# Optimization experiments

Hardware: AMD Instinct MI355X
Metric: run time of the kernel (lower is better)

## Reference

```python
import jax, jax.numpy as jnp
import numpy as np

N = 10000           # nodes
E = 160000          # edges
MUL = 128           # multiplicity of each irrep (128x0e + 128x1o)
EDGE_FEAT = 8       # radial embedding dim
AVG_NUM_NEIGHBORS = 16.0
MLP_IN = MUL + MUL + EDGE_FEAT + 1  # 265
NUM_W = 4 * MUL     # irreps_mid num_irreps = 256x0e + 256x1o -> 512 path weights
SQ3 = float(np.sqrt(3.0))


def setup_inputs() -> dict:
    key = jax.random.key(0)
    ks = jax.random.split(key, 16)
    node_feats = jax.random.normal(ks[0], (N, 4 * MUL), dtype=jnp.float32)  # [N,512] = 128x0e ++ 128x1o
    edge_attrs = jax.random.normal(ks[1], (E, 4), dtype=jnp.float32)        # 1x0e ++ 1x1o
    edge_feats = jax.random.normal(ks[2], (E, EDGE_FEAT), dtype=jnp.float32)
    lengths = jax.random.uniform(ks[3], (E, 1), dtype=jnp.float32)
    edge_index = jax.random.randint(ks[4], (2, E), 0, N, dtype=jnp.int32)
    # e3nn Linear weights (stored unit-variance; forward applies 1/sqrt(fan_in))
    W_scalar = jax.random.normal(ks[5], (MUL, MUL), dtype=jnp.float32)
    W_up0 = jax.random.normal(ks[6], (MUL, MUL), dtype=jnp.float32)
    W_up1 = jax.random.normal(ks[7], (MUL, MUL), dtype=jnp.float32)
    # conv_tp_weights MLP (flax Dense: fan-scaled init, bias on first two layers)
    W1 = jax.random.normal(ks[8], (MLP_IN, MUL), dtype=jnp.float32) / np.sqrt(MLP_IN)
    b1 = jnp.zeros((MUL,), dtype=jnp.float32)
    W2 = jax.random.normal(ks[9], (MUL, MUL), dtype=jnp.float32) / np.sqrt(MUL)
    b2 = jnp.zeros((MUL,), dtype=jnp.float32)
    W3 = jax.random.normal(ks[10], (MUL, NUM_W), dtype=jnp.float32) / np.sqrt(MUL)
    # final e3nn Linear: 256x0e+256x1o -> 128x0e+128x1o
    Wout0 = jax.random.normal(ks[11], (2 * MUL, MUL), dtype=jnp.float32)
    Wout1 = jax.random.normal(ks[12], (2 * MUL, MUL), dtype=jnp.float32)
    return {"node_feats": node_feats, "edge_attrs": edge_attrs, "edge_feats": edge_feats,
            "lengths": lengths, "edge_index": edge_index, "W_scalar": W_scalar,
            "W_up0": W_up0, "W_up1": W_up1, "W1": W1, "b1": b1, "W2": W2, "b2": b2,
            "W3": W3, "Wout0": Wout0, "Wout1": Wout1}


def reference(node_feats, edge_attrs, edge_feats, lengths, edge_index,
              W_scalar, W_up0, W_up1, W1, b1, W2, b2, W3, Wout0, Wout1):
    n = node_feats.shape[0]
    inv = 1.0 / np.sqrt(MUL)
    x0 = node_feats[:, :MUL]                       # [N,128]   0e
    x1 = node_feats[:, MUL:].reshape(n, MUL, 3)    # [N,128,3] 1o

    # linear_scalar: only 0e->0e path survives
    scalars = (x0 @ W_scalar) * inv                # [N,128]
    # linear_up: per-irrep channel mixing
    h0 = (x0 @ W_up0) * inv                        # [N,128]
    h1 = jnp.einsum('nmi,mo->noi', x1, W_up1) * inv  # [N,128,3]

    sender, receiver = edge_index[0], edge_index[1]

    # conv_tp_weights MLP
    mlp_in = jnp.concatenate([scalars[sender], scalars[receiver], edge_feats, lengths], axis=-1)
    h = jax.nn.silu(mlp_in @ W1 + b1)
    h = jax.nn.silu(h @ W2 + b2)
    tpw = h @ W3                                   # [E,512]

    xs0 = h0[sender]                               # [E,128]
    xs1 = h1[sender]                               # [E,128,3]
    y0 = edge_attrs[:, 0:1]                        # [E,1]  0e
    y1 = edge_attrs[:, 1:4]                        # [E,3]  1o

    # CG tensor product (component normalization), filtered to {0e,1o}; sorted order:
    # 0e block = [0e*0e->0e, 1o*1o->0e], 1o block = [0e*1o->1o, 1o*0e->1o]
    mA = xs0 * y0                                       # [E,128]   0e
    mD = (xs1 * y1[:, None, :]).sum(-1) / SQ3           # [E,128]   0e
    mB = xs0[:, :, None] * y1[:, None, :]               # [E,128,3] 1o
    mC = xs1 * y0[:, :, None]                           # [E,128,3] 1o

    # per-irrep path weights (one scalar per irrep channel)
    wA, wD = tpw[:, :MUL], tpw[:, MUL:2 * MUL]
    wB, wC = tpw[:, 2 * MUL:3 * MUL], tpw[:, 3 * MUL:]

    m0 = jnp.concatenate([mA * wA, mD * wD], axis=1)                          # [E,256]
    m1 = jnp.concatenate([mB * wB[:, :, None], mC * wC[:, :, None]], axis=1)  # [E,256,3]

    # scatter-sum aggregation to receivers
    agg0 = jax.ops.segment_sum(m0, receiver, num_segments=n)  # [N,256]
    agg1 = jax.ops.segment_sum(m1, receiver, num_segments=n)  # [N,256,3]

    # final e3nn Linear + / avg_num_neighbors
    scale = 1.0 / (np.sqrt(2 * MUL) * AVG_NUM_NEIGHBORS)
    out0 = (agg0 @ Wout0) * scale                             # [N,128]
    out1 = jnp.einsum('nmi,mo->noi', agg1, Wout1) * scale     # [N,128,3]

    # reshape_irreps: [N, mul, sum(ir dims)] = [N,128,4]
    return jnp.concatenate([out0[:, :, None], out1], axis=-1)
```

## Files before the change

### kernel.cpp

```cpp
#include <hip/hip_runtime.h>
#include <hip/hip_bf16.h>

#define NN 10000
#define NE 160000
#define TILE 32
#define A1S 264
#define A2S 136

typedef __attribute__((ext_vector_type(8))) short short8;
typedef __attribute__((ext_vector_type(4))) float f32x4;

__device__ __forceinline__ float silu_f(float x) { return x / (1.0f + __expf(-x)); }
__device__ __forceinline__ unsigned short bf16u(float v) {
    __hip_bfloat16 b = __float2bfloat16(v);
    return *reinterpret_cast<unsigned short*>(&b);
}
__device__ __forceinline__ short8 pack8(float4 a, float4 b) {
    short8 r;
    r[0]=(short)bf16u(a.x); r[1]=(short)bf16u(a.y); r[2]=(short)bf16u(a.z); r[3]=(short)bf16u(a.w);
    r[4]=(short)bf16u(b.x); r[5]=(short)bf16u(b.y); r[6]=(short)bf16u(b.z); r[7]=(short)bf16u(b.w);
    return r;
}
__device__ __forceinline__ void lds_barrier() {
    asm volatile("s_waitcnt lgkmcnt(0)" ::: "memory");
    __builtin_amdgcn_s_barrier();
    asm volatile("" ::: "memory");
}

#define OFF_W1  0
#define OFF_W2  36864
#define OFF_W3  53248
#define OFF_WSC 118784
#define OFF_WU0 135168
#define OFF_WU1 151552
#define OFF_WO0 167936
#define OFF_WO1 200704
#define WP_TOTAL 233472

__global__ __launch_bounds__(256) void convert_weights(
    const float* __restrict__ W1, const float* __restrict__ W2,
    const float* __restrict__ W3, const float* __restrict__ Wsc,
    const float* __restrict__ Wu0, const float* __restrict__ Wu1,
    const float* __restrict__ Wo0, const float* __restrict__ Wo1,
    unsigned short* __restrict__ wp,
    const int* __restrict__ edge_index, int* __restrict__ deg)
{
    int idx = blockIdx.x * 256 + threadIdx.x;
    if (idx < NE) atomicAdd(&deg[edge_index[NE + idx]], 1);
    if (idx >= WP_TOTAL) return;
    const float* src; int off, N, K;
    if      (idx < OFF_W2)  { src = W1;  off = OFF_W1;  N = 128; K = 265; }
    else if (idx < OFF_W3)  { src = W2;  off = OFF_W2;  N = 128; K = 128; }
    else if (idx < OFF_WSC) { src = W3;  off = OFF_W3;  N = 512; K = 128; }
    else if (idx < OFF_WU0) { src = Wsc; off = OFF_WSC; N = 128; K = 128; }
    else if (idx < OFF_WU1) { src = Wu0; off = OFF_WU0; N = 128; K = 128; }
    else if (idx < OFF_WO0) { src = Wu1; off = OFF_WU1; N = 128; K = 128; }
    else if (idx < OFF_WO1) { src = Wo0; off = OFF_WO0; N = 128; K = 256; }
    else                    { src = Wo1; off = OFF_WO1; N = 128; K = 256; }
    int j = idx - off;
    int kt = j / (N * 32);
    int rem = j % (N * 32);
    int n = rem >> 5, kk = rem & 31;
    int k = kt * 32 + kk;
    wp[idx] = (k < K) ? bf16u(src[k * N + n]) : (unsigned short)0;
}

__global__ __launch_bounds__(256) void node_transform(
    const float* __restrict__ node_feats,
    const unsigned short* __restrict__ wp,
    unsigned short* __restrict__ scalars_bf,
    unsigned short* __restrict__ hall,
    float* __restrict__ agg0, float* __restrict__ agg1t)
{
    __shared__ unsigned short xls[4 * 16 * 136];
    const int t = threadIdx.x;
    const int bn = blockIdx.x * 16;

    {
        const float4 z = make_float4(0.f, 0.f, 0.f, 0.f);
        float4* a0 = (float4*)(agg0 + (size_t)bn * 256);
        #pragma unroll
        for (int i = 0; i < 4; ++i) a0[t + 256 * i] = z;
        #pragma unroll
        for (int c = 0; c < 3; ++c) {
            float4* a1 = (float4*)(agg1t + (size_t)c * NN * 256 + (size_t)bn * 256);
            #pragma unroll
            for (int i = 0; i < 4; ++i) a1[t + 256 * i] = z;
        }
    }

    for (int i = t; i < 16 * 512; i += 256) {
        int n = i >> 9, j = i & 511;
        unsigned short u = bf16u(node_feats[(size_t)(bn + n) * 512 + j]);
        if (j < 128) xls[n * 136 + j] = u;
        else {
            int jj = j - 128;
            int m = jj / 3;
            int c = jj - 3 * m;
            xls[(1 + c) * 2176 + n * 136 + m] = u;
        }
    }
    __syncthreads();

    const int wv = t >> 6, lane = t & 63, l16 = lane & 15, l4 = lane >> 4;
    const unsigned short* Wscp = wp + OFF_WSC;
    const unsigned short* Wu0p = wp + OFF_WU0;
    const unsigned short* Wu1p = wp + OFF_WU1;

    f32x4 asc[2] = {}, ah0[2] = {}, ah1[3][2] = {};
    for (int kt = 0; kt < 4; ++kt) {
        short8 ax0 = *(const short8*)(xls + l16 * 136 + kt * 32 + l4 * 8);
        short8 ax1[3];
        #pragma unroll
        for (int c = 0; c < 3; ++c)
            ax1[c] = *(const short8*)(xls + (1 + c) * 2176 + l16 * 136 + kt * 32 + l4 * 8);
        #pragma unroll
        for (int n = 0; n < 2; ++n) {
            int col = wv * 32 + n * 16 + l16;
            short8 bsc = *(const short8*)(Wscp + ((size_t)kt * 128 + col) * 32 + l4 * 8);
            short8 bu0 = *(const short8*)(Wu0p + ((size_t)kt * 128 + col) * 32 + l4 * 8);
            short8 bu1 = *(const short8*)(Wu1p + ((size_t)kt * 128 + col) * 32 + l4 * 8);
            asc[n] = __builtin_amdgcn_mfma_f32_16x16x32_bf16(ax0, bsc, asc[n], 0, 0, 0);
            ah0[n] = __builtin_amdgcn_mfma_f32_16x16x32_bf16(ax0, bu0, ah0[n], 0, 0, 0);
            #pragma unroll
            for (int c = 0; c < 3; ++c)
                ah1[c][n] = __builtin_amdgcn_mfma_f32_16x16x32_bf16(ax1[c], bu1, ah1[c][n], 0, 0, 0);
        }
    }
    const float inv = 0.08838834764831845f;
    #pragma unroll
    for (int n = 0; n < 2; ++n) {
        int col = wv * 32 + n * 16 + l16;
        #pragma unroll
        for (int r = 0; r < 4; ++r) {
            int node = bn + l4 * 4 + r;
            scalars_bf[(size_t)node * 128 + col] = bf16u(asc[n][r] * inv);
            unsigned int lo = (unsigned int)bf16u(ah0[n][r] * inv)
                            | ((unsigned int)bf16u(ah1[0][n][r] * inv) << 16);
            unsigned int hi = (unsigned int)bf16u(ah1[1][n][r] * inv)
                            | ((unsigned int)bf16u(ah1[2][n][r] * inv) << 16);
            *(uint2*)(hall + ((size_t)node * 128 + col) * 4) = make_uint2(lo, hi);
        }
    }
}

__global__ __launch_bounds__(1024) void scan_kernel(const int* __restrict__ deg,
                                                    int* __restrict__ cursor) {
    __shared__ int s[1024];
    const int t = threadIdx.x;
    const int base = t * 10;
    int ld[10];
    int lsum = 0;
    #pragma unroll
    for (int i = 0; i < 10; ++i) {
        int idx = base + i;
        ld[i] = (idx < NN) ? deg[idx] : 0;
        lsum += ld[i];
    }
    s[t] = lsum;
    __syncthreads();
    for (int off = 1; off < 1024; off <<= 1) {
        int u = (t >= off) ? s[t - off] : 0;
        __syncthreads();
        s[t] += u;
        __syncthreads();
    }
    int run = s[t] - lsum;
    #pragma unroll
    for (int i = 0; i < 10; ++i) {
        int idx = base + i;
        if (idx < NN) cursor[idx] = run;
        run += ld[i];
    }
}

__global__ __launch_bounds__(256) void perm_kernel(const int* __restrict__ edge_index,
                                                   int* __restrict__ cursor,
                                                   int* __restrict__ perm) {
    int e = blockIdx.x * 256 + threadIdx.x;
    if (e < NE) {
        int r = edge_index[NE + e];
        int pos = atomicAdd(&cursor[r], 1);
        perm[pos] = e;
    }
}

__global__ __launch_bounds__(256, 6) void edge_kernel(
    const unsigned short* __restrict__ scalars_bf,
    const unsigned short* __restrict__ hall,
    const float* __restrict__ edge_attrs,
    const float* __restrict__ edge_feats,
    const float* __restrict__ lengths,
    const int* __restrict__ edge_index,
    const int* __restrict__ perm,
    const float* __restrict__ b1, const float* __restrict__ b2,
    const unsigned short* __restrict__ wp,
    float* __restrict__ agg0, float* __restrict__ agg1t)
{
    __shared__ unsigned char smem_u[25600];
    __shared__ int   eid_s[TILE];
    __shared__ int   s_s[TILE];
    __shared__ int   r_s[TILE];
    __shared__ float4 y_s[TILE];

    unsigned short* A1 = (unsigned short*)smem_u;
    unsigned short* A2 = (unsigned short*)(smem_u + 16896);
    unsigned short* A3 = A1;
    float* PKh = (float*)(smem_u + 8704);

    const int t = threadIdx.x;
    const int e0 = blockIdx.x * TILE;
    const int wv = t >> 6;
    const int lane = t & 63;
    const int l16 = lane & 15;
    const int l4 = lane >> 4;

    if (t < TILE) {
        int eid = perm[e0 + t];
        eid_s[t] = eid;
        s_s[t] = edge_index[eid];
        r_s[t] = edge_index[NE + eid];
        y_s[t] = *(const float4*)(edge_attrs + (size_t)eid * 4);
    }
    __syncthreads();

    {
        const int e = t >> 3, j = t & 7;
        const unsigned short* srow = scalars_bf + (size_t)s_s[e] * 128;
        const unsigned short* rrow = scalars_bf + (size_t)r_s[e] * 128;
        *(uint4*)(A1 + e*A1S + j*16)       = *(const uint4*)(srow + j*16);
        *(uint4*)(A1 + e*A1S + j*16 + 8)   = *(const uint4*)(srow + j*16 + 8);
        *(uint4*)(A1 + e*A1S + 128 + j*16)     = *(const uint4*)(rrow + j*16);
        *(uint4*)(A1 + e*A1S + 128 + j*16 + 8) = *(const uint4*)(rrow + j*16 + 8);
    }

    short8 ef0 = (short8){0,0,0,0,0,0,0,0}, ef1 = ef0;
    {
        int eA = l16, eB = 16 + l16;
        if (l4 == 0) {
            float4 v0 = *(const float4*)(edge_feats + (size_t)eid_s[eA] * 8);
            float4 v1 = *(const float4*)(edge_feats + (size_t)eid_s[eA] * 8 + 4);
            ef0 = pack8(v0, v1);
            float4 u0 = *(const float4*)(edge_feats + (size_t)eid_s[eB] * 8);
            float4 u1 = *(const float4*)(edge_feats + (size_t)eid_s[eB] * 8 + 4);
            ef1 = pack8(u0, u1);
        } else if (l4 == 1) {
            ef0[0] = (short)bf16u(lengths[eid_s[eA]]);
            ef1[0] = (short)bf16u(lengths[eid_s[eB]]);
        }
    }

    const int q = t >> 6, o = t & 63;
    const int rlo = q * 8;
    uint2 pfA[8], pfB[8];
    #pragma unroll
    for (int i = 0; i < 8; ++i)
        pfA[i] = *(const uint2*)(hall + ((size_t)s_s[rlo + i] * 128 + o) * 4);
    __syncthreads();

    const unsigned short* Wp1 = wp + OFF_W1;
    const unsigned short* Wp2 = wp + OFF_W2;
    const unsigned short* Wp3 = wp + OFF_W3;

    {
        f32x4 acc[2][2] = {};
        for (int kt = 0; kt < 8; ++kt) {
            short8 a0 = *(const short8*)(A1 + (     l16)*A1S + kt*32 + l4*8);
            short8 a1 = *(const short8*)(A1 + (16 + l16)*A1S + kt*32 + l4*8);
            #pragma unroll
            for (int n = 0; n < 2; ++n) {
                int col = (2*wv + n)*16 + l16;
                short8 b = *(const short8*)(Wp1 + ((size_t)kt*128 + col)*32 + l4*8);
                acc[0][n] = __builtin_amdgcn_mfma_f32_16x16x32_bf16(a0, b, acc[0][n], 0, 0, 0);
                acc[1][n] = __builtin_amdgcn_mfma_f32_16x16x32_bf16(a1, b, acc[1][n], 0, 0, 0);
            }
        }
        {
            #pragma unroll
            for (int n = 0; n < 2; ++n) {
                int col = (2*wv + n)*16 + l16;
                short8 b = *(const short8*)(Wp1 + ((size_t)8*128 + col)*32 + l4*8);
                acc[0][n] = __builtin_amdgcn_mfma_f32_16x16x32_bf16(ef0, b, acc[0][n], 0, 0, 0);
                acc[1][n] = __builtin_amdgcn_mfma_f32_16x16x32_bf16(ef1, b, acc[1][n], 0, 0, 0);
            }
        }
        #pragma unroll
        for (int n = 0; n < 2; ++n) {
            int col = (2*wv + n)*16 + l16;
            float bb = b1[col];
            #pragma unroll
            for (int m = 0; m < 2; ++m)
                #pragma unroll
                for (int r = 0; r < 4; ++r) {
                    int row = m*16 + l4*4 + r;
                    A2[row*A2S + col] = bf16u(silu_f(acc[m][n][r] + bb));
                }
        }
    }
    __syncthreads();

    {
        f32x4 acc[2][2] = {};
        for (int kt = 0; kt < 4; ++kt) {
            short8 a0 = *(const short8*)(A2 + (     l16)*A2S + kt*32 + l4*8);
            short8 a1 = *(const short8*)(A2 + (16 + l16)*A2S + kt*32 + l4*8);
            #pragma unroll
            for (int n = 0; n < 2; ++n) {
                int col = (2*wv + n)*16 + l16;
                short8 b = *(const short8*)(Wp2 + ((size_t)kt*128 + col)*32 + l4*8);
                acc[0][n] = __builtin_amdgcn_mfma_f32_16x16x32_bf16(a0, b, acc[0][n], 0, 0, 0);
                acc[1][n] = __builtin_amdgcn_mfma_f32_16x16x32_bf16(a1, b, acc[1][n], 0, 0, 0);
            }
        }
        #pragma unroll
        for (int n = 0; n < 2; ++n) {
            int col = (2*wv + n)*16 + l16;
            float bb = b2[col];
            #pragma unroll
            for (int m = 0; m < 2; ++m)
                #pragma unroll
                for (int r = 0; r < 4; ++r) {
                    int row = m*16 + l4*4 + r;
                    A3[row*A2S + col] = bf16u(silu_f(acc[m][n][r] + bb));
                }
        }
    }
    __syncthreads();

    const float rs3 = 0.57735026918962576f;
    auto do_seg = [&](const int pass, const int hh, const uint2* pf) {
        const int base0 = pass ? 128 : 0;
        const int base1 = pass ? 384 : 256;
        f32x4 acc[2][2] = {};
        for (int kt = 0; kt < 4; ++kt) {
            short8 a0 = *(const short8*)(A3 + (     l16)*A2S + kt*32 + l4*8);
            short8 a1 = *(const short8*)(A3 + (16 + l16)*A2S + kt*32 + l4*8);
            #pragma unroll
            for (int fam = 0; fam < 2; ++fam) {
                int col = (fam ? base1 : base0) + hh*64 + wv*16 + l16;
                short8 b = *(const short8*)(Wp3 + ((size_t)kt*512 + col)*32 + l4*8);
                acc[fam][0] = __builtin_amdgcn_mfma_f32_16x16x32_bf16(a0, b, acc[fam][0], 0, 0, 0);
                acc[fam][1] = __builtin_amdgcn_mfma_f32_16x16x32_bf16(a1, b, acc[fam][1], 0, 0, 0);
            }
        }
        #pragma unroll
        for (int fam = 0; fam < 2; ++fam)
            #pragma unroll
            for (int m = 0; m < 2; ++m)
                #pragma unroll
                for (int r = 0; r < 4; ++r) {
                    int row = m*16 + l4*4 + r;
                    float y0 = y_s[row].x;
                    float fold = (fam == 0) ? (pass ? rs3 : y0) : (pass ? y0 : 1.0f);
                    PKh[row*132 + fam*64 + wv*16 + l16] = acc[fam][m][r] * fold;
                }
        lds_barrier();

        {
            const int ocol = hh*64 + o;
            float ac0 = 0.f, ac1 = 0.f, ac2 = 0.f, ac3 = 0.f;
            int run_start = rlo;
            int prev_rn = r_s[rlo];

            auto flush = [&](int rn, bool interior) {
                size_t b0 = (size_t)rn * 256 + base0 + ocol;
                if (interior) {
                    agg0[b0] = ac0;
                    agg1t[0*(size_t)NN*256 + b0] = ac1;
                    agg1t[1*(size_t)NN*256 + b0] = ac2;
                    agg1t[2*(size_t)NN*256 + b0] = ac3;
                } else {
                    atomicAdd(agg0 + b0, ac0);
                    atomicAdd(agg1t + 0*(size_t)NN*256 + b0, ac1);
                    atomicAdd(agg1t + 1*(size_t)NN*256 + b0, ac2);
                    atomicAdd(agg1t + 2*(size_t)NN*256 + b0, ac3);
                }
            };

            #pragma unroll
            for (int i = 0; i < 8; ++i) {
                int row = rlo + i;
                int rn = r_s[row];
                if (rn != prev_rn) {
                    flush(prev_rn, run_start > rlo);
                    ac0 = ac1 = ac2 = ac3 = 0.f;
                    run_start = row;
                    prev_rn = rn;
                }
                float w0 = PKh[row*132 + o];
                float w1 = PKh[row*132 + 64 + o];
                float4 y = y_s[row];
                if (pass == 0) {
                    float x = __uint_as_float(pf[i].x << 16);
                    ac0 = fmaf(x, w0, ac0);
                    float xb = x * w1;
                    ac1 = fmaf(xb, y.y, ac1);
                    ac2 = fmaf(xb, y.z, ac2);
                    ac3 = fmaf(xb, y.w, ac3);
                } else {
                    float xx = __uint_as_float(pf[i].x & 0xffff0000u);
                    float xy = __uint_as_float(pf[i].y << 16);
                    float xz = __uint_as_float(pf[i].y & 0xffff0000u);
                    float dd = xx*y.y + xy*y.z + xz*y.w;
                    ac0 = fmaf(dd, w0, ac0);
                    ac1 = fmaf(xx, w1, ac1);
                    ac2 = fmaf(xy, w1, ac2);
                    ac3 = fmaf(xz, w1, ac3);
                }
            }
            flush(prev_rn, false);
        }
        lds_barrier();
    };

    do_seg(0, 0, pfA);
    do_seg(1, 0, pfA);
    #pragma unroll
    for (int i = 0; i < 8; ++i)
        pfB[i] = *(const uint2*)(hall + ((size_t)s_s[rlo + i] * 128 + 64 + o) * 4);
    do_seg(0, 1, pfB);
    do_seg(1, 1, pfB);
}

__global__ __launch_bounds__(256) void output_transform(
    const float* __restrict__ agg0,
    const float* __restrict__ agg1t,
    const unsigned short* __restrict__ wp,
    float* __restrict__ out)
{
    __shared__ unsigned short As[4][16 * 264];
    const int t = threadIdx.x;
    const int bn = blockIdx.x * 16;

    for (int i = t; i < 2048; i += 256) {
        int mat = i >> 9;
        int rem = i & 511;
        int n = rem >> 5;
        int ko = (rem & 31) * 8;
        const float* src = (mat == 0)
            ? (agg0 + (size_t)(bn + n) * 256 + ko)
            : (agg1t + (size_t)(mat - 1) * NN * 256 + (size_t)(bn + n) * 256 + ko);
        float4 v0 = *(const float4*)(src);
        float4 v1 = *(const float4*)(src + 4);
        *(short8*)(&As[mat][n * 264 + ko]) = pack8(v0, v1);
    }
    __syncthreads();

    const int wv = t >> 6, lane = t & 63, l16 = lane & 15, l4 = lane >> 4;
    const unsigned short* Wo0p = wp + OFF_WO0;
    const unsigned short* Wo1p = wp + OFF_WO1;

    f32x4 acc[2][4] = {};
    for (int kt = 0; kt < 8; ++kt) {
        short8 a0 = *(const short8*)(&As[0][l16 * 264 + kt * 32 + l4 * 8]);
        short8 a1 = *(const short8*)(&As[1][l16 * 264 + kt * 32 + l4 * 8]);
        short8 a2 = *(const short8*)(&As[2][l16 * 264 + kt * 32 + l4 * 8]);
        short8 a3 = *(const short8*)(&As[3][l16 * 264 + kt * 32 + l4 * 8]);
        #pragma unroll
        for (int n = 0; n < 2; ++n) {
            int col = wv * 32 + n * 16 + l16;
            short8 bw0 = *(const short8*)(Wo0p + ((size_t)kt * 128 + col) * 32 + l4 * 8);
            short8 bw1 = *(const short8*)(Wo1p + ((size_t)kt * 128 + col) * 32 + l4 * 8);
            acc[n][0] = __builtin_amdgcn_mfma_f32_16x16x32_bf16(a0, bw0, acc[n][0], 0, 0, 0);
            acc[n][1] = __builtin_amdgcn_mfma_f32_16x16x32_bf16(a1, bw1, acc[n][1], 0, 0, 0);
            acc[n][2] = __builtin_amdgcn_mfma_f32_16x16x32_bf16(a2, bw1, acc[n][2], 0, 0, 0);
            acc[n][3] = __builtin_amdgcn_mfma_f32_16x16x32_bf16(a3, bw1, acc[n][3], 0, 0, 0);
        }
    }
    const float scale = 0.00390625f;
    #pragma unroll
    for (int n = 0; n < 2; ++n) {
        int col = wv * 32 + n * 16 + l16;
        #pragma unroll
        for (int r = 0; r < 4; ++r) {
            int node = bn + l4 * 4 + r;
            float4 v = make_float4(acc[n][0][r] * scale, acc[n][1][r] * scale,
                                   acc[n][2][r] * scale, acc[n][3][r] * scale);
            *(float4*)(out + ((size_t)node * 128 + col) * 4) = v;
        }
    }
}

extern "C" void kernel_launch(void* const* d_in, const int* in_sizes, int n_in,
                              void* d_out, int out_size, void* d_ws, size_t ws_size,
                              hipStream_t stream) {
    const float* node_feats = (const float*)d_in[0];
    const float* edge_attrs = (const float*)d_in[1];
    const float* edge_feats = (const float*)d_in[2];
    const float* lengths    = (const float*)d_in[3];
    const int*   edge_index = (const int*)d_in[4];
    const float* W_scalar   = (const float*)d_in[5];
    const float* W_up0      = (const float*)d_in[6];
    const float* W_up1      = (const float*)d_in[7];
    const float* W1         = (const float*)d_in[8];
    const float* b1         = (const float*)d_in[9];
    const float* W2         = (const float*)d_in[10];
    const float* b2         = (const float*)d_in[11];
    const float* W3         = (const float*)d_in[12];
    const float* Wout0      = (const float*)d_in[13];
    const float* Wout1      = (const float*)d_in[14];

    float* ws = (float*)d_ws;
    unsigned short* scalars_bf = (unsigned short*)ws;
    unsigned short* hall = (unsigned short*)(ws + 640000);
    float* agg0  = ws + 3200000;
    float* agg1t = ws + 5760000;
    int* deg    = (int*)(ws + 13440000);
    int* cursor = (int*)(ws + 13450000);
    int* perm   = (int*)(ws + 13460000);
    unsigned short* wpack = (unsigned short*)(ws + 13620000);
    if (ws_size < 13736736ull * 4ull) return;

    hipMemsetAsync(deg, 0, NN * 4, stream);
    convert_weights<<<(WP_TOTAL + 255) / 256, 256, 0, stream>>>(
        W1, W2, W3, W_scalar, W_up0, W_up1, Wout0, Wout1, wpack, edge_index, deg);
    node_transform<<<625, 256, 0, stream>>>(node_feats, wpack, scalars_bf, hall, agg0, agg1t);
    scan_kernel<<<1, 1024, 0, stream>>>(deg, cursor);
    perm_kernel<<<(NE + 255) / 256, 256, 0, stream>>>(edge_index, cursor, perm);
    edge_kernel<<<NE / TILE, 256, 0, stream>>>(scalars_bf, hall, edge_attrs, edge_feats, lengths,
                                               edge_index, perm, b1, b2, wpack, agg0, agg1t);
    output_transform<<<625, 256, 0, stream>>>(agg0, agg1t, wpack, (float*)d_out);
}
```

Measured before the change: 219.2 us.

## Process two edge tiles per block and prefetch the second tile's gathers

The edge kernel now handles two 32-edge tiles per block. While the first tile runs its MLP and scatter work, the second tile's indices, scalar rows, edge features and hall gathers are issued into registers early, so global-load latency overlaps with MFMA and atomic work. Grid size halves and the launch-bounds occupancy hint drops from 6 to 5 to fit the extra live registers. The risks are lower occupancy, higher register pressure, and fewer blocks to balance across CUs.

```diff
diff --git a/kernel.cpp b/kernel.cpp
--- a/kernel.cpp
+++ b/kernel.cpp
@@ -185,7 +185,7 @@
     }
 }
 
-__global__ __launch_bounds__(256, 6) void edge_kernel(
+__global__ __launch_bounds__(256, 5) void edge_kernel(
     const unsigned short* __restrict__ scalars_bf,
     const unsigned short* __restrict__ hall,
     const float* __restrict__ edge_attrs,
@@ -198,10 +198,10 @@
     float* __restrict__ agg0, float* __restrict__ agg1t)
 {
     __shared__ unsigned char smem_u[25600];
-    __shared__ int   eid_s[TILE];
-    __shared__ int   s_s[TILE];
-    __shared__ int   r_s[TILE];
-    __shared__ float4 y_s[TILE];
+    __shared__ int   eid_s[2][TILE];
+    __shared__ int   s_s[2][TILE];
+    __shared__ int   r_s[2][TILE];
+    __shared__ float4 y_s[2][TILE];
 
     unsigned short* A1 = (unsigned short*)smem_u;
     unsigned short* A2 = (unsigned short*)(smem_u + 16896);
@@ -209,60 +209,21 @@
     float* PKh = (float*)(smem_u + 8704);
 
     const int t = threadIdx.x;
-    const int e0 = blockIdx.x * TILE;
+    const int e0 = blockIdx.x * (2 * TILE);
     const int wv = t >> 6;
     const int lane = t & 63;
     const int l16 = lane & 15;
     const int l4 = lane >> 4;
-
-    if (t < TILE) {
-        int eid = perm[e0 + t];
-        eid_s[t] = eid;
-        s_s[t] = edge_index[eid];
-        r_s[t] = edge_index[NE + eid];
-        y_s[t] = *(const float4*)(edge_attrs + (size_t)eid * 4);
-    }
-    __syncthreads();
-
-    {
-        const int e = t >> 3, j = t & 7;
-        const unsigned short* srow = scalars_bf + (size_t)s_s[e] * 128;
-        const unsigned short* rrow = scalars_bf + (size_t)r_s[e] * 128;
-        *(uint4*)(A1 + e*A1S + j*16)       = *(const uint4*)(srow + j*16);
-        *(uint4*)(A1 + e*A1S + j*16 + 8)   = *(const uint4*)(srow + j*16 + 8);
-        *(uint4*)(A1 + e*A1S + 128 + j*16)     = *(const uint4*)(rrow + j*16);
-        *(uint4*)(A1 + e*A1S + 128 + j*16 + 8) = *(const uint4*)(rrow + j*16 + 8);
-    }
-
-    short8 ef0 = (short8){0,0,0,0,0,0,0,0}, ef1 = ef0;
-    {
-        int eA = l16, eB = 16 + l16;
-        if (l4 == 0) {
-            float4 v0 = *(const float4*)(edge_feats + (size_t)eid_s[eA] * 8);
-            float4 v1 = *(const float4*)(edge_feats + (size_t)eid_s[eA] * 8 + 4);
-            ef0 = pack8(v0, v1);
-            float4 u0 = *(const float4*)(edge_feats + (size_t)eid_s[eB] * 8);
-            float4 u1 = *(const float4*)(edge_feats + (size_t)eid_s[eB] * 8 + 4);
-            ef1 = pack8(u0, u1);
-        } else if (l4 == 1) {
-            ef0[0] = (short)bf16u(lengths[eid_s[eA]]);
-            ef1[0] = (short)bf16u(lengths[eid_s[eB]]);
-        }
-    }
-
     const int q = t >> 6, o = t & 63;
     const int rlo = q * 8;
-    uint2 pfA[8], pfB[8];
-    #pragma unroll
-    for (int i = 0; i < 8; ++i)
-        pfA[i] = *(const uint2*)(hall + ((size_t)s_s[rlo + i] * 128 + o) * 4);
-    __syncthreads();
+    const int es = t >> 3, j8 = t & 7;
 
     const unsigned short* Wp1 = wp + OFF_W1;
     const unsigned short* Wp2 = wp + OFF_W2;
     const unsigned short* Wp3 = wp + OFF_W3;
-
-    {
+    const float rs3 = 0.57735026918962576f;
+
+    auto do_L1 = [&](short8 efa, short8 efb) {
         f32x4 acc[2][2] = {};
         for (int kt = 0; kt < 8; ++kt) {
             short8 a0 = *(const short8*)(A1 + (     l16)*A1S + kt*32 + l4*8);
@@ -280,8 +241,8 @@
             for (int n = 0; n < 2; ++n) {
                 int col = (2*wv + n)*16 + l16;
                 short8 b = *(const short8*)(Wp1 + ((size_t)8*128 + col)*32 + l4*8);
-                acc[0][n] = __builtin_amdgcn_mfma_f32_16x16x32_bf16(ef0, b, acc[0][n], 0, 0, 0);
-                acc[1][n] = __builtin_amdgcn_mfma_f32_16x16x32_bf16(ef1, b, acc[1][n], 0, 0, 0);
+                acc[0][n] = __builtin_amdgcn_mfma_f32_16x16x32_bf16(efa, b, acc[0][n], 0, 0, 0);
+                acc[1][n] = __builtin_amdgcn_mfma_f32_16x16x32_bf16(efb, b, acc[1][n], 0, 0, 0);
             }
         }
         #pragma unroll
@@ -296,10 +257,9 @@
                     A2[row*A2S + col] = bf16u(silu_f(acc[m][n][r] + bb));
                 }
         }
-    }
-    __syncthreads();
-
-    {
+    };
+
+    auto do_L2 = [&]() {
         f32x4 acc[2][2] = {};
         for (int kt = 0; kt < 4; ++kt) {
             short8 a0 = *(const short8*)(A2 + (     l16)*A2S + kt*32 + l4*8);
@@ -324,11 +284,10 @@
                     A3[row*A2S + col] = bf16u(silu_f(acc[m][n][r] + bb));
                 }
         }
-    }
-    __syncthreads();
-
-    const float rs3 = 0.57735026918962576f;
-    auto do_seg = [&](const int pass, const int hh, const uint2* pf) {
+    };
+
+    auto do_seg = [&](const int pass, const int hh, const uint2* pf,
+                      const int* rs, const float4* ys) {
         const int base0 = pass ? 128 : 0;
         const int base1 = pass ? 384 : 256;
         f32x4 acc[2][2] = {};
@@ -350,7 +309,7 @@
                 #pragma unroll
                 for (int r = 0; r < 4; ++r) {
                     int row = m*16 + l4*4 + r;
-                    float y0 = y_s[row].x;
+                    float y0 = ys[row].x;
                     float fold = (fam == 0) ? (pass ? rs3 : y0) : (pass ? y0 : 1.0f);
                     PKh[row*132 + fam*64 + wv*16 + l16] = acc[fam][m][r] * fold;
                 }
@@ -360,7 +319,7 @@
             const int ocol = hh*64 + o;
             float ac0 = 0.f, ac1 = 0.f, ac2 = 0.f, ac3 = 0.f;
             int run_start = rlo;
-            int prev_rn = r_s[rlo];
+            int prev_rn = rs[rlo];
 
             auto flush = [&](int rn, bool interior) {
                 size_t b0 = (size_t)rn * 256 + base0 + ocol;
@@ -380,7 +339,7 @@
             #pragma unroll
             for (int i = 0; i < 8; ++i) {
                 int row = rlo + i;
-                int rn = r_s[row];
+                int rn = rs[row];
                 if (rn != prev_rn) {
                     flush(prev_rn, run_start > rlo);
                     ac0 = ac1 = ac2 = ac3 = 0.f;
@@ -389,7 +348,7 @@
                 }
                 float w0 = PKh[row*132 + o];
                 float w1 = PKh[row*132 + 64 + o];
-                float4 y = y_s[row];
+                float4 y = ys[row];
                 if (pass == 0) {
                     float x = __uint_as_float(pf[i].x << 16);
                     ac0 = fmaf(x, w0, ac0);
@@ -413,13 +372,124 @@
         lds_barrier();
     };
 
-    do_seg(0, 0, pfA);
-    do_seg(1, 0, pfA);
+    if (t < TILE) {
+        int eid = perm[e0 + t];
+        eid_s[0][t] = eid;
+        s_s[0][t] = edge_index[eid];
+        r_s[0][t] = edge_index[NE + eid];
+        y_s[0][t] = *(const float4*)(edge_attrs + (size_t)eid * 4);
+    }
+    __syncthreads();
+
+    {
+        const unsigned short* srow = scalars_bf + (size_t)s_s[0][es] * 128;
+        const unsigned short* rrow = scalars_bf + (size_t)r_s[0][es] * 128;
+        *(uint4*)(A1 + es*A1S + j8*16)       = *(const uint4*)(srow + j8*16);
+        *(uint4*)(A1 + es*A1S + j8*16 + 8)   = *(const uint4*)(srow + j8*16 + 8);
+        *(uint4*)(A1 + es*A1S + 128 + j8*16)     = *(const uint4*)(rrow + j8*16);
+        *(uint4*)(A1 + es*A1S + 128 + j8*16 + 8) = *(const uint4*)(rrow + j8*16 + 8);
+    }
+    short8 efa0 = (short8){0,0,0,0,0,0,0,0}, efb0 = efa0;
+    {
+        int eA = l16, eB = 16 + l16;
+        if (l4 == 0) {
+            float4 v0 = *(const float4*)(edge_feats + (size_t)eid_s[0][eA] * 8);
+            float4 v1 = *(const float4*)(edge_feats + (size_t)eid_s[0][eA] * 8 + 4);
+            efa0 = pack8(v0, v1);
+            float4 u0 = *(const float4*)(edge_feats + (size_t)eid_s[0][eB] * 8);
+            float4 u1 = *(const float4*)(edge_feats + (size_t)eid_s[0][eB] * 8 + 4);
+            efb0 = pack8(u0, u1);
+        } else if (l4 == 1) {
+            efa0[0] = (short)bf16u(lengths[eid_s[0][eA]]);
+            efb0[0] = (short)bf16u(lengths[eid_s[0][eB]]);
+        }
+    }
+    uint2 pfA0[8];
     #pragma unroll
     for (int i = 0; i < 8; ++i)
-        pfB[i] = *(const uint2*)(hall + ((size_t)s_s[rlo + i] * 128 + 64 + o) * 4);
-    do_seg(0, 1, pfB);
-    do_seg(1, 1, pfB);
+        pfA0[i] = *(const uint2*)(hall + ((size_t)s_s[0][rlo + i] * 128 + o) * 4);
+    __syncthreads();
+
+    int h_eid = 0, h_s = 0, h_r = 0; float4 h_y = make_float4(0,0,0,0);
+    if (t < TILE) {
+        h_eid = perm[e0 + TILE + t];
+        h_s = edge_index[h_eid];
+        h_r = edge_index[NE + h_eid];
+        h_y = *(const float4*)(edge_attrs + (size_t)h_eid * 4);
+    }
+
+    do_L1(efa0, efb0);
+    __syncthreads();
+    do_L2();
+    if (t < TILE) {
+        eid_s[1][t] = h_eid; s_s[1][t] = h_s; r_s[1][t] = h_r; y_s[1][t] = h_y;
+    }
+    __syncthreads();
+
+    uint4 nsv0, nsv1, nrv0, nrv1;
+    {
+        const unsigned short* srow = scalars_bf + (size_t)s_s[1][es] * 128;
+        const unsigned short* rrow = scalars_bf + (size_t)r_s[1][es] * 128;
+        nsv0 = *(const uint4*)(srow + j8*16);
+        nsv1 = *(const uint4*)(srow + j8*16 + 8);
+        nrv0 = *(const uint4*)(rrow + j8*16);
+        nrv1 = *(const uint4*)(rrow + j8*16 + 8);
+    }
+    float4 nva0 = make_float4(0,0,0,0), nva1 = nva0, nvb0 = nva0, nvb1 = nva0;
+    float nla = 0.f, nlb = 0.f;
+    {
+        int eA = l16, eB = 16 + l16;
+        if (l4 == 0) {
+            nva0 = *(const float4*)(edge_feats + (size_t)eid_s[1][eA] * 8);
+            nva1 = *(const float4*)(edge_feats + (size_t)eid_s[1][eA] * 8 + 4);
+            nvb0 = *(const float4*)(edge_feats + (size_t)eid_s[1][eB] * 8);
+            nvb1 = *(const float4*)(edge_feats + (size_t)eid_s[1][eB] * 8 + 4);
+        } else if (l4 == 1) {
+            nla = lengths[eid_s[1][eA]];
+            nlb = lengths[eid_s[1][eB]];
+        }
+    }
+
+    do_seg(0, 0, pfA0, &r_s[0][0], &y_s[0][0]);
+    do_seg(1, 0, pfA0, &r_s[0][0], &y_s[0][0]);
+    uint2 pfN[8];
+    #pragma unroll
+    for (int i = 0; i < 8; ++i)
+        pfN[i] = *(const uint2*)(hall + ((size_t)s_s[1][rlo + i] * 128 + o) * 4);
+    uint2 pfB0[8];
+    #pragma unroll
+    for (int i = 0; i < 8; ++i)
+        pfB0[i] = *(const uint2*)(hall + ((size_t)s_s[0][rlo + i] * 128 + 64 + o) * 4);
+    do_seg(0, 1, pfB0, &r_s[0][0], &y_s[0][0]);
+    do_seg(1, 1, pfB0, &r_s[0][0], &y_s[0][0]);
+
+    *(uint4*)(A1 + es*A1S + j8*16)       = nsv0;
+    *(uint4*)(A1 + es*A1S + j8*16 + 8)   = nsv1;
+    *(uint4*)(A1 + es*A1S + 128 + j8*16)     = nrv0;
+    *(uint4*)(A1 + es*A1S + 128 + j8*16 + 8) = nrv1;
+    short8 efa1 = (short8){0,0,0,0,0,0,0,0}, efb1 = efa1;
+    if (l4 == 0) {
+        efa1 = pack8(nva0, nva1);
+        efb1 = pack8(nvb0, nvb1);
+    } else if (l4 == 1) {
+        efa1[0] = (short)bf16u(nla);
+        efb1[0] = (short)bf16u(nlb);
+    }
+    lds_barrier();
+
+    do_L1(efa1, efb1);
+    lds_barrier();
+    do_L2();
+    lds_barrier();
+
+    do_seg(0, 0, pfN, &r_s[1][0], &y_s[1][0]);
+    do_seg(1, 0, pfN, &r_s[1][0], &y_s[1][0]);
+    uint2 pfB1[8];
+    #pragma unroll
+    for (int i = 0; i < 8; ++i)
+        pfB1[i] = *(const uint2*)(hall + ((size_t)s_s[1][rlo + i] * 128 + 64 + o) * 4);
+    do_seg(0, 1, pfB1, &r_s[1][0], &y_s[1][0]);
+    do_seg(1, 1, pfB1, &r_s[1][0], &y_s[1][0]);
 }
 
 __global__ __launch_bounds__(256) void output_transform(
@@ -517,7 +587,7 @@
     node_transform<<<625, 256, 0, stream>>>(node_feats, wpack, scalars_bf, hall, agg0, agg1t);
     scan_kernel<<<1, 1024, 0, stream>>>(deg, cursor);
     perm_kernel<<<(NE + 255) / 256, 256, 0, stream>>>(edge_index, cursor, perm);
-    edge_kernel<<<NE / TILE, 256, 0, stream>>>(scalars_bf, hall, edge_attrs, edge_feats, lengths,
-                                               edge_index, perm, b1, b2, wpack, agg0, agg1t);
+    edge_kernel<<<NE / (2 * TILE), 256, 0, stream>>>(scalars_bf, hall, edge_attrs, edge_feats, lengths,
+                                                     edge_index, perm, b1, b2, wpack, agg0, agg1t);
     output_transform<<<625, 256, 0, stream>>>(agg0, agg1t, wpack, (float*)d_out);
 }
```

Result: slower. 316.7 us (+44.5%).
